# Performance work log

Hardware: AMD Instinct MI355X
Metric: run time of the kernel (lower is better)

## Reference

```python
import jax, jax.numpy as jnp
import numpy as np

N = 50000
E = 500000
D = 512


def setup_inputs() -> dict:
    key = jax.random.key(0)
    ks = jax.random.split(key, 16)
    inp = {
        'h': jax.random.normal(ks[0], (N, D), jnp.float32),
        's': jax.random.normal(ks[1], (N, D), jnp.float32),
        'm': jax.random.normal(ks[2], (N, D), jnp.float32),
        'norm_g': jax.random.uniform(ks[3], (N, 1), jnp.float32),
        'norm_f': jax.random.uniform(ks[4], (N, 1), jnp.float32),
        'src_g': jax.random.randint(ks[5], (E,), 0, N, jnp.int32),
        'dst_g': jax.random.randint(ks[6], (E,), 0, N, jnp.int32),
        'src_f': jax.random.randint(ks[7], (E,), 0, N, jnp.int32),
        'dst_f': jax.random.randint(ks[8], (E,), 0, N, jnp.int32),
        'wh': jax.random.normal(ks[9], (D, D), jnp.float32) / np.sqrt(D),
        'ws': jax.random.normal(ks[10], (D, D), jnp.float32) / np.sqrt(D),
        'wm': jax.random.normal(ks[11], (D, D), jnp.float32) / np.sqrt(D),
        'bh': jax.random.normal(ks[12], (D,), jnp.float32) * 0.02,
        'bs': jax.random.normal(ks[13], (D,), jnp.float32) * 0.02,
        'bm': jax.random.normal(ks[14], (D,), jnp.float32) * 0.02,
    }
    return inp


def reference(h, s, m, norm_g, norm_f, src_g, dst_g, src_f, dst_f, wh, ws, wm, bh, bs, bm):
    n = h.shape[0]
    # dense projections
    h = (h @ wh) * norm_g          # [N,D]
    s = (s @ ws) * norm_f          # [N,D]
    m = m @ wm                     # [N,D] global skip
    # dual GCN aggregation: copy_src + sum over edges, then norm scaling
    h = jax.ops.segment_sum(h[src_g], dst_g, num_segments=n) * norm_g
    s = jax.ops.segment_sum(s[src_f], dst_f, num_segments=n) * norm_f
    # bias add + three-way residual sum + activation
    out = (h + bh) + (s + bs) + (m + bm)
    return jax.nn.relu(out)
```

## Files before the change

### kernel.cpp

```cpp
#include <hip/hip_runtime.h>
#include <hip/hip_bf16.h>
#include <cstdint>
#include <cstddef>

#define DD 512
#define D4 128

typedef unsigned short u16;
typedef unsigned int u32;
typedef short s8v __attribute__((ext_vector_type(8)));
typedef float f4v __attribute__((ext_vector_type(4)));

__device__ __forceinline__ u16 f2bf(float f) {
  u32 u = __builtin_bit_cast(u32, f);
  u = (u + 0x7FFFu + ((u >> 16) & 1u)) >> 16;
  return (u16)u;
}
__device__ __forceinline__ float bf2f(u16 h) {
  u32 u = ((u32)h) << 16;
  return __builtin_bit_cast(float, u);
}

__device__ __forceinline__ void glds16(const void* g, void* l) {
  __builtin_amdgcn_global_load_lds(
      (const __attribute__((address_space(1))) void*)g,
      (__attribute__((address_space(3))) void*)l, 16, 0, 0);
}


__global__ void hist_kernel(const int* __restrict__ dg, const int* __restrict__ df,
                            int* __restrict__ deg_g, int* __restrict__ deg_f, int E) {
  int i = blockIdx.x * blockDim.x + threadIdx.x;
  int total = 2 * E;
  int stride = gridDim.x * blockDim.x;
  for (; i < total; i += stride) {
    if (i < E) atomicAdd(&deg_g[dg[i]], 1);
    else       atomicAdd(&deg_f[df[i - E]], 1);
  }
}

__global__ void scan_kernel(const int* __restrict__ deg_g, const int* __restrict__ deg_f,
                            int* __restrict__ rp_g, int* __restrict__ rp_f,
                            int* __restrict__ cur_g, int* __restrict__ cur_f, int N) {
  const int* deg = (blockIdx.x == 0) ? deg_g : deg_f;
  int* rp  = (blockIdx.x == 0) ? rp_g  : rp_f;
  int* cur = (blockIdx.x == 0) ? cur_g : cur_f;
  __shared__ int sums[256];
  int t = threadIdx.x;
  int strip = (N + 255) / 256;
  int base = t * strip;
  int lim = N - base; if (lim > strip) lim = strip; if (lim < 0) lim = 0;
  int s = 0;
  for (int j = 0; j < lim; ++j) s += deg[base + j];
  sums[t] = s;
  __syncthreads();
  for (int off = 1; off < 256; off <<= 1) {
    int v = sums[t];
    int add = (t >= off) ? sums[t - off] : 0;
    __syncthreads();
    sums[t] = v + add;
    __syncthreads();
  }
  int run = (t == 0) ? 0 : sums[t - 1];
  for (int j = 0; j < lim; ++j) {
    rp[base + j] = run;
    cur[base + j] = run;
    run += deg[base + j];
  }
  if (t == 255) rp[N] = sums[255];
}

__global__ void fill_kernel(const int* __restrict__ src, const int* __restrict__ dst,
                            int* __restrict__ cur, int* __restrict__ csr, int E) {
  int i = blockIdx.x * blockDim.x + threadIdx.x;
  int stride = gridDim.x * blockDim.x;
  for (; i < E; i += stride) {
    int d = dst[i];
    int pos = atomicAdd(&cur[d], 1);
    csr[pos] = src[i];
  }
}


__global__ __launch_bounds__(128) void gather_kernel(const float* __restrict__ feat,
    const float* __restrict__ norm, const int* __restrict__ rp, const int* __restrict__ csr,
    float* __restrict__ X, int N) {
  int i = blockIdx.x;
  if (i >= N) return;
  int c = threadIdx.x;
  const float4* f4 = (const float4*)feat;
  float4 acc = make_float4(0.f, 0.f, 0.f, 0.f);
  int b = rp[i], e = rp[i + 1];
  for (int j = b; j < e; ++j) {
    int s = csr[j];
    float gs = norm[s];
    float4 v = f4[(size_t)s * D4 + c];
    acc.x += gs * v.x; acc.y += gs * v.y; acc.z += gs * v.z; acc.w += gs * v.w;
  }
  float gi = norm[i];
  float4 o = make_float4(acc.x * gi, acc.y * gi, acc.z * gi, acc.w * gi);
  ((float4*)X)[(size_t)i * D4 + c] = o;
}


__global__ __launch_bounds__(256) void wsplit_kernel(
    const float* __restrict__ wh, const float* __restrict__ ws, const float* __restrict__ wm,
    u16* __restrict__ WtHi, u16* __restrict__ WtLo) {
  __shared__ float tile[64][65];
  int si = blockIdx.y;
  const float* W = (si == 0) ? wh : (si == 1) ? ws : wm;
  int tb = blockIdx.x;
  int kb = (tb >> 3) << 6;
  int cb = (tb & 7) << 6;
  int t = threadIdx.x;
#pragma unroll
  for (int i = 0; i < 16; ++i) {
    int idx = t + (i << 8);
    int kr = idx >> 6, cc = idx & 63;
    tile[kr][cc] = W[(size_t)(kb + kr) * DD + cb + cc];
  }
  __syncthreads();
  size_t base = (size_t)si * DD * DD;
#pragma unroll
  for (int i = 0; i < 16; ++i) {
    int idx = t + (i << 8);
    int cr = idx >> 6, kk = idx & 63;
    float v = tile[kk][cr];
    u16 hi = f2bf(v);
    u16 lo = f2bf(v - bf2f(hi));
    size_t off = base + (size_t)(cb + cr) * DD + kb + kk;
    WtHi[off] = hi;
    WtLo[off] = lo;
  }
}


#define BM 128
#define BN 256
#define BK 32

__global__ __launch_bounds__(256, 2) void gemm3_mfma(
    const float* __restrict__ Xh, const float* __restrict__ Xs, const float* __restrict__ Mm,
    const u16* __restrict__ WtHi, const u16* __restrict__ WtLo,
    const float* __restrict__ bh, const float* __restrict__ bs, const float* __restrict__ bm,
    float* __restrict__ out, int Mrows) {
  __shared__ u16 sAh[BM * BK];
  __shared__ u16 sAl[BM * BK];
  __shared__ u16 sBh[BN * BK];
  __shared__ u16 sBl[BN * BK];

  int tid = threadIdx.x;
  int wv = tid >> 6;
  int lane = tid & 63;
  int bm0 = blockIdx.y * BM;
  int bn0 = blockIdx.x * BN;

  f4v acc[8][4];
#pragma unroll
  for (int i = 0; i < 8; ++i)
#pragma unroll
    for (int j = 0; j < 4; ++j) acc[i][j] = (f4v){0.f, 0.f, 0.f, 0.f};

  const float* Aarr[3] = {Xh, Xs, Mm};

  for (int si = 0; si < 3; ++si) {
    const float* A = Aarr[si];
    const u16* WH = WtHi + (size_t)si * DD * DD;
    const u16* WL = WtLo + (size_t)si * DD * DD;
    for (int k0 = 0; k0 < DD; k0 += BK) {
      {
        int colo = lane >> 2;
        int chunk = lane & 3;
#pragma unroll
        for (int i = 0; i < 4; ++i) {
          int cg = wv * 4 + i;
          int col = cg * 16 + colo;
          const u16* gh = WH + (size_t)(bn0 + col) * DD + k0 + chunk * 8;
          const u16* gl = WL + (size_t)(bn0 + col) * DD + k0 + chunk * 8;
          glds16(gh, (char*)sBh + cg * 1024);
          glds16(gl, (char*)sBl + cg * 1024);
        }
      }
      {
        float4 vv[4];
#pragma unroll
        for (int i = 0; i < 4; ++i) {
          int idx = tid + (i << 8);
          int row = idx >> 3;
          int gr = bm0 + row;
          int kc = idx & 7;
          vv[i] = make_float4(0.f, 0.f, 0.f, 0.f);
          if (gr < Mrows) vv[i] = *(const float4*)(A + (size_t)gr * DD + k0 + kc * 4);
        }
#pragma unroll
        for (int i = 0; i < 4; ++i) {
          int idx = tid + (i << 8);
          int row = idx >> 3;
          int kc = idx & 7;
          float4 v = vv[i];
          u16 h0 = f2bf(v.x), h1 = f2bf(v.y), h2 = f2bf(v.z), h3 = f2bf(v.w);
          u16 l0 = f2bf(v.x - bf2f(h0)), l1 = f2bf(v.y - bf2f(h1));
          u16 l2 = f2bf(v.z - bf2f(h2)), l3 = f2bf(v.w - bf2f(h3));
          uint2 ph = make_uint2((u32)h0 | ((u32)h1 << 16), (u32)h2 | ((u32)h3 << 16));
          uint2 pl = make_uint2((u32)l0 | ((u32)l1 << 16), (u32)l2 | ((u32)l3 << 16));
          *(uint2*)(sAh + row * BK + kc * 4) = ph;
          *(uint2*)(sAl + row * BK + kc * 4) = pl;
        }
      }
      __syncthreads();
      int kchunk = (lane >> 4) * 8;
      int rr = lane & 15;
      s8v bhf[4], blf[4];
#pragma unroll
      for (int ng = 0; ng < 4; ++ng) {
        int col = wv * 64 + ng * 16 + rr;
        bhf[ng] = *(const s8v*)(sBh + col * BK + kchunk);
        blf[ng] = *(const s8v*)(sBl + col * BK + kchunk);
      }
#pragma unroll
      for (int mg = 0; mg < 8; ++mg) {
        int row = mg * 16 + rr;
        s8v ah = *(const s8v*)(sAh + row * BK + kchunk);
        s8v al = *(const s8v*)(sAl + row * BK + kchunk);
#pragma unroll
        for (int ng = 0; ng < 4; ++ng) {
          acc[mg][ng] = __builtin_amdgcn_mfma_f32_16x16x32_bf16(ah, bhf[ng], acc[mg][ng], 0, 0, 0);
          acc[mg][ng] = __builtin_amdgcn_mfma_f32_16x16x32_bf16(al, bhf[ng], acc[mg][ng], 0, 0, 0);
          acc[mg][ng] = __builtin_amdgcn_mfma_f32_16x16x32_bf16(ah, blf[ng], acc[mg][ng], 0, 0, 0);
        }
      }
      __syncthreads();
    }
  }

  int rr = lane & 15;
  int rgrp = lane >> 4;
  float bias[4];
#pragma unroll
  for (int ng = 0; ng < 4; ++ng) {
    int col = bn0 + wv * 64 + ng * 16 + rr;
    bias[ng] = bh[col] + bs[col] + bm[col];
  }
#pragma unroll
  for (int mg = 0; mg < 8; ++mg) {
#pragma unroll
    for (int r = 0; r < 4; ++r) {
      int row = bm0 + mg * 16 + rgrp * 4 + r;
      if (row < Mrows) {
#pragma unroll
        for (int ng = 0; ng < 4; ++ng) {
          int col = bn0 + wv * 64 + ng * 16 + rr;
          float v = acc[mg][ng][r] + bias[ng];
          out[(size_t)row * DD + col] = v > 0.f ? v : 0.f;
        }
      }
    }
  }
}


extern "C" void kernel_launch(void* const* d_in, const int* in_sizes, int n_in,
                              void* d_out, int out_size, void* d_ws, size_t ws_size,
                              hipStream_t stream) {
  const float* h   = (const float*)d_in[0];
  const float* s   = (const float*)d_in[1];
  const float* m   = (const float*)d_in[2];
  const float* ng  = (const float*)d_in[3];
  const float* nf  = (const float*)d_in[4];
  const int* src_g = (const int*)d_in[5];
  const int* dst_g = (const int*)d_in[6];
  const int* src_f = (const int*)d_in[7];
  const int* dst_f = (const int*)d_in[8];
  const float* wh  = (const float*)d_in[9];
  const float* wsp = (const float*)d_in[10];
  const float* wm  = (const float*)d_in[11];
  const float* bh  = (const float*)d_in[12];
  const float* bs  = (const float*)d_in[13];
  const float* bm  = (const float*)d_in[14];
  float* out = (float*)d_out;

  int N = in_sizes[3];
  int E = in_sizes[5];

  float* Xh = (float*)d_ws;
  float* Xs = Xh + (size_t)N * DD;
  u16* WtHi = (u16*)(Xs + (size_t)N * DD);
  u16* WtLo = WtHi + (size_t)3 * DD * DD;
  int* deg_g = (int*)(WtLo + (size_t)3 * DD * DD);
  int* deg_f = deg_g + N;
  int* rp_g  = deg_f + N;
  int* rp_f  = rp_g + (N + 1);
  int* cur_g = rp_f + (N + 1);
  int* cur_f = cur_g + N;
  int* csr_g = cur_f + N;
  int* csr_f = csr_g + E;

  hipMemsetAsync(deg_g, 0, 2 * (size_t)N * sizeof(int), stream);
  wsplit_kernel<<<dim3(64, 3), 256, 0, stream>>>(wh, wsp, wm, WtHi, WtLo);
  hist_kernel<<<2048, 256, 0, stream>>>(dst_g, dst_f, deg_g, deg_f, E);
  scan_kernel<<<2, 256, 0, stream>>>(deg_g, deg_f, rp_g, rp_f, cur_g, cur_f, N);
  fill_kernel<<<2048, 256, 0, stream>>>(src_g, dst_g, cur_g, csr_g, E);
  fill_kernel<<<2048, 256, 0, stream>>>(src_f, dst_f, cur_f, csr_f, E);
  gather_kernel<<<N, 128, 0, stream>>>(h, ng, rp_g, csr_g, Xh, N);
  gather_kernel<<<N, 128, 0, stream>>>(s, nf, rp_f, csr_f, Xs, N);

  dim3 gg(DD / BN, (N + BM - 1) / BM);
  gemm3_mfma<<<gg, 256, 0, stream>>>(Xh, Xs, m, WtHi, WtLo, bh, bs, bm, out, N);
}
```

Measured before the change: 1.170 ms.

## Emit bf16 hi/lo split from gather and stream it into GEMM via LDS loads

The gather kernels now split their aggregated rows into bf16 hi/lo pairs and write those instead of fp32. The GEMM loads the two aggregated operands straight into LDS with global_load_lds, so it no longer converts them to bf16 inside its k-loop. The gather loop is also unrolled by four to keep more independent row loads in flight. Workspace rows are padded to a multiple of BM so the unguarded async loads stay in bounds. The padding rows are never written, so those tiles read uninitialized memory, though only into output rows that are masked.

```diff
diff --git a/kernel.cpp b/kernel.cpp
--- a/kernel.cpp
+++ b/kernel.cpp
@@ -84,22 +84,40 @@
 
 __global__ __launch_bounds__(128) void gather_kernel(const float* __restrict__ feat,
     const float* __restrict__ norm, const int* __restrict__ rp, const int* __restrict__ csr,
-    float* __restrict__ X, int N) {
+    u16* __restrict__ XHi, u16* __restrict__ XLo, int N) {
   int i = blockIdx.x;
   if (i >= N) return;
   int c = threadIdx.x;
   const float4* f4 = (const float4*)feat;
   float4 acc = make_float4(0.f, 0.f, 0.f, 0.f);
   int b = rp[i], e = rp[i + 1];
-  for (int j = b; j < e; ++j) {
+  int j = b;
+  for (; j + 4 <= e; j += 4) {
+    int s0 = csr[j], s1 = csr[j + 1], s2 = csr[j + 2], s3 = csr[j + 3];
+    float g0 = norm[s0], g1 = norm[s1], g2 = norm[s2], g3 = norm[s3];
+    float4 v0 = f4[(size_t)s0 * D4 + c];
+    float4 v1 = f4[(size_t)s1 * D4 + c];
+    float4 v2 = f4[(size_t)s2 * D4 + c];
+    float4 v3 = f4[(size_t)s3 * D4 + c];
+    acc.x += g0 * v0.x + g1 * v1.x + g2 * v2.x + g3 * v3.x;
+    acc.y += g0 * v0.y + g1 * v1.y + g2 * v2.y + g3 * v3.y;
+    acc.z += g0 * v0.z + g1 * v1.z + g2 * v2.z + g3 * v3.z;
+    acc.w += g0 * v0.w + g1 * v1.w + g2 * v2.w + g3 * v3.w;
+  }
+  for (; j < e; ++j) {
     int s = csr[j];
     float gs = norm[s];
     float4 v = f4[(size_t)s * D4 + c];
     acc.x += gs * v.x; acc.y += gs * v.y; acc.z += gs * v.z; acc.w += gs * v.w;
   }
   float gi = norm[i];
-  float4 o = make_float4(acc.x * gi, acc.y * gi, acc.z * gi, acc.w * gi);
-  ((float4*)X)[(size_t)i * D4 + c] = o;
+  float o0 = acc.x * gi, o1 = acc.y * gi, o2 = acc.z * gi, o3 = acc.w * gi;
+  u16 h0 = f2bf(o0), h1 = f2bf(o1), h2 = f2bf(o2), h3 = f2bf(o3);
+  ushort4 hv = make_ushort4(h0, h1, h2, h3);
+  ushort4 lv = make_ushort4(f2bf(o0 - bf2f(h0)), f2bf(o1 - bf2f(h1)),
+                            f2bf(o2 - bf2f(h2)), f2bf(o3 - bf2f(h3)));
+  *(ushort4*)(XHi + (size_t)i * DD + c * 4) = hv;
+  *(ushort4*)(XLo + (size_t)i * DD + c * 4) = lv;
 }
 
 
@@ -140,7 +158,9 @@
 #define BK 32
 
 __global__ __launch_bounds__(256, 2) void gemm3_mfma(
-    const float* __restrict__ Xh, const float* __restrict__ Xs, const float* __restrict__ Mm,
+    const u16* __restrict__ XhHi, const u16* __restrict__ XhLo,
+    const u16* __restrict__ XsHi, const u16* __restrict__ XsLo,
+    const float* __restrict__ Mm,
     const u16* __restrict__ WtHi, const u16* __restrict__ WtLo,
     const float* __restrict__ bh, const float* __restrict__ bs, const float* __restrict__ bm,
     float* __restrict__ out, int Mrows) {
@@ -161,10 +181,9 @@
 #pragma unroll
     for (int j = 0; j < 4; ++j) acc[i][j] = (f4v){0.f, 0.f, 0.f, 0.f};
 
-  const float* Aarr[3] = {Xh, Xs, Mm};
-
   for (int si = 0; si < 3; ++si) {
-    const float* A = Aarr[si];
+    const u16* AH = (si == 0) ? XhHi : XsHi;
+    const u16* AL = (si == 0) ? XhLo : XsLo;
     const u16* WH = WtHi + (size_t)si * DD * DD;
     const u16* WL = WtLo + (size_t)si * DD * DD;
     for (int k0 = 0; k0 < DD; k0 += BK) {
@@ -181,7 +200,19 @@
           glds16(gl, (char*)sBl + cg * 1024);
         }
       }
-      {
+      if (si < 2) {
+        int rowo = lane >> 2;
+        int chunk = lane & 3;
+#pragma unroll
+        for (int i = 0; i < 2; ++i) {
+          int rg = wv * 2 + i;
+          int row = rg * 16 + rowo;
+          const u16* gh = AH + (size_t)(bm0 + row) * DD + k0 + chunk * 8;
+          const u16* gl = AL + (size_t)(bm0 + row) * DD + k0 + chunk * 8;
+          glds16(gh, (char*)sAh + rg * 1024);
+          glds16(gl, (char*)sAl + rg * 1024);
+        }
+      } else {
         float4 vv[4];
 #pragma unroll
         for (int i = 0; i < 4; ++i) {
@@ -190,7 +221,7 @@
           int gr = bm0 + row;
           int kc = idx & 7;
           vv[i] = make_float4(0.f, 0.f, 0.f, 0.f);
-          if (gr < Mrows) vv[i] = *(const float4*)(A + (size_t)gr * DD + k0 + kc * 4);
+          if (gr < Mrows) vv[i] = *(const float4*)(Mm + (size_t)gr * DD + k0 + kc * 4);
         }
 #pragma unroll
         for (int i = 0; i < 4; ++i) {
@@ -281,10 +312,13 @@
 
   int N = in_sizes[3];
   int E = in_sizes[5];
-
-  float* Xh = (float*)d_ws;
-  float* Xs = Xh + (size_t)N * DD;
-  u16* WtHi = (u16*)(Xs + (size_t)N * DD);
+  int Npad = (N + BM - 1) & ~(BM - 1);
+
+  u16* XhHi = (u16*)d_ws;
+  u16* XhLo = XhHi + (size_t)Npad * DD;
+  u16* XsHi = XhLo + (size_t)Npad * DD;
+  u16* XsLo = XsHi + (size_t)Npad * DD;
+  u16* WtHi = XsLo + (size_t)Npad * DD;
   u16* WtLo = WtHi + (size_t)3 * DD * DD;
   int* deg_g = (int*)(WtLo + (size_t)3 * DD * DD);
   int* deg_f = deg_g + N;
@@ -301,9 +335,10 @@
   scan_kernel<<<2, 256, 0, stream>>>(deg_g, deg_f, rp_g, rp_f, cur_g, cur_f, N);
   fill_kernel<<<2048, 256, 0, stream>>>(src_g, dst_g, cur_g, csr_g, E);
   fill_kernel<<<2048, 256, 0, stream>>>(src_f, dst_f, cur_f, csr_f, E);
-  gather_kernel<<<N, 128, 0, stream>>>(h, ng, rp_g, csr_g, Xh, N);
-  gather_kernel<<<N, 128, 0, stream>>>(s, nf, rp_f, csr_f, Xs, N);
+  gather_kernel<<<N, 128, 0, stream>>>(h, ng, rp_g, csr_g, XhHi, XhLo, N);
+  gather_kernel<<<N, 128, 0, stream>>>(s, nf, rp_f, csr_f, XsHi, XsLo, N);
 
   dim3 gg(DD / BN, (N + BM - 1) / BM);
-  gemm3_mfma<<<gg, 256, 0, stream>>>(Xh, Xs, m, WtHi, WtLo, bh, bs, bm, out, N);
-}
+  gemm3_mfma<<<gg, 256, 0, stream>>>(XhHi, XhLo, XsHi, XsLo, m, WtHi, WtLo,
+                                     bh, bs, bm, out, N);
+}
```

New measurement: 1.095 ms. 6.4% less time.
